# Optimization experiments

Hardware: AMD Instinct MI355X
Metric: run time of the kernel (lower is better)

## Reference

```python
import jax, jax.numpy as jnp
import numpy as np

IMG = 256      # image size implied by 8x8 grid * scale 32
THRE = 0.5
DIS = 4        # img_dislocate_size
B = 64


def _shift_map(s, size, dis):
    # Pixel-level coordinate map for the dislocated half: cell r starts at
    # max(r*s - dis, 0) (the torch while-loop clamps negative coords to 0).
    p = jnp.arange(size)
    base = jnp.maximum((p // s) * s - dis, 0)
    return base + p % s


def _cell_norm(x, g, s):
    # Per-cell (crop) min/max normalization, matching the per-crop
    # (t - min) / (max - min + 1e-5) in HeatMaptoImg.
    b = x.shape[0]
    v = x.reshape(b, 1, g, s, g, s)
    mn = v.min(axis=(3, 5), keepdims=True)
    mx = v.max(axis=(3, 5), keepdims=True)
    return ((v - mn) / (mx - mn + 1e-5)).reshape(b, 1, g * s, g * s)


def setup_inputs() -> dict:
    key = jax.random.key(0)
    ks = jax.random.split(key, 7)
    B2 = 2 * B
    return {
        "img": jax.random.uniform(ks[0], (B, 1, IMG, IMG), jnp.float32),
        "heat8": jax.random.uniform(ks[1], (B2, 1, 8, 8), jnp.float32),
        "heat16": jax.random.uniform(ks[2], (B2, 1, 16, 16), jnp.float32),
        "heat32": jax.random.uniform(ks[3], (B2, 1, 32, 32), jnp.float32),
        "seg8": jax.random.uniform(ks[4], (B2, 1, IMG, IMG), jnp.float32),
        "seg16": jax.random.uniform(ks[5], (B2, 1, IMG, IMG), jnp.float32),
        "seg32": jax.random.uniform(ks[6], (B2, 1, IMG, IMG), jnp.float32),
    }


def reference(img, heat8, heat16, heat32, seg8, seg16, seg32):
    Bv = img.shape[0]
    label = jnp.zeros((Bv, 1, IMG, IMG), img.dtype)
    cnt = jnp.zeros_like(label)
    crops = {}
    # fine grid (scale 8) processed first, matching the reversed loop order
    for heat, seg, g in ((heat32, seg32, 32), (heat16, seg16, 16), (heat8, seg8, 8)):
        s = IMG // g                      # crop / cell size for this scale
        mask = (heat > THRE).astype(img.dtype)          # (2B,1,g,g)
        mask_pix = jnp.repeat(jnp.repeat(mask, s, axis=2), s, axis=3)  # (2B,1,256,256)
        Y = _shift_map(s, IMG, DIS)
        # dislocated half crops come from the shifted image region
        img_d = img[:, :, Y[:, None], Y[None, :]]       # (B,1,256,256)
        both = jnp.concatenate([img, img_d], axis=0)    # (2B,1,256,256)
        crops[g] = _cell_norm(both, g, s) * mask_pix
        # UnitLabels: scatter-add per-crop labels + counts, then average
        ca = mask_pix[:Bv]
        label = label + ca * seg[:Bv]
        cnt = cnt + ca
        cd = mask_pix[Bv:]
        label = label.at[:, :, Y[:, None], Y[None, :]].add(cd * seg[Bv:])
        cnt = cnt.at[:, :, Y[:, None], Y[None, :]].add(cd)
    label = label / (cnt + 1e-10)
    return (crops[32], crops[16], crops[8], label)
```

## Files before the change

### kernel.cpp

```cpp
#include <hip/hip_runtime.h>

#define IMG   256
#define IMG2  65536
#define NB    64
#define NB2   128

#define NBLK_C8   2048
#define NBLK_C16  1024
#define NBLK_C32  512
#define NBLK_LBL  4096
#define NBLK_ALL  (NBLK_C8 + NBLK_C16 + NBLK_C32 + NBLK_LBL)

template <int S>
__device__ __forceinline__ void crops_cell_row(
    const float* __restrict__ img,
    const float* __restrict__ heat,
    float* __restrict__ out,
    int src, int ci,
    float (*s_red)[32][4],
    float (*s_fin)[4]) {
    constexpr int G   = IMG / S;
    constexpr int L   = (S == 8) ? 3 : (S == 16) ? 4 : 5;
    constexpr int CPL = S / 4;

    const int tid = threadIdx.x;
    const int w   = tid >> 6;
    const int l   = tid & 63;
    const int cj  = l >> (L - 2);
    const int o   = (l & (CPL - 1)) * 4;

    const int rA   = ci * S;
    const int rB   = (ci == 0) ? 0 : rA - 4;
    const int colA = cj * S + o;
    const int colB = ((cj == 0) ? 0 : cj * S - 4) + o;

    const float* __restrict__ sp = img + (size_t)src * IMG2;

    float mnA = 3.4e38f, mxA = -3.4e38f, mnB = 3.4e38f, mxB = -3.4e38f;
#pragma unroll
    for (int k = 0; k < S / 4; ++k) {
        const int r = w + 4 * k;
        const float4 a  = *(const float4*)(sp + (rA + r) * IMG + colA);
        const float4 bq = *(const float4*)(sp + (rB + r) * IMG + colB);
        mnA = fminf(mnA, fminf(fminf(a.x, a.y), fminf(a.z, a.w)));
        mxA = fmaxf(mxA, fmaxf(fmaxf(a.x, a.y), fmaxf(a.z, a.w)));
        mnB = fminf(mnB, fminf(fminf(bq.x, bq.y), fminf(bq.z, bq.w)));
        mxB = fmaxf(mxB, fmaxf(fmaxf(bq.x, bq.y), fmaxf(bq.z, bq.w)));
    }
#pragma unroll
    for (int off = 1; off < CPL; off <<= 1) {
        mnA = fminf(mnA, __shfl_xor(mnA, off, 64));
        mxA = fmaxf(mxA, __shfl_xor(mxA, off, 64));
        mnB = fminf(mnB, __shfl_xor(mnB, off, 64));
        mxB = fmaxf(mxB, __shfl_xor(mxB, off, 64));
    }
    if ((l & (CPL - 1)) == 0) {
        float* p = &s_red[w][cj][0];
        p[0] = mnA; p[1] = mxA; p[2] = mnB; p[3] = mxB;
    }
    __syncthreads();
    if (tid < G) {
        float a0 = 3.4e38f, a1 = -3.4e38f, b0 = 3.4e38f, b1 = -3.4e38f;
#pragma unroll
        for (int ww = 0; ww < 4; ++ww) {
            a0 = fminf(a0, s_red[ww][tid][0]);
            a1 = fmaxf(a1, s_red[ww][tid][1]);
            b0 = fminf(b0, s_red[ww][tid][2]);
            b1 = fmaxf(b1, s_red[ww][tid][3]);
        }
        const float hA = heat[(size_t)src * G * G + ci * G + tid];
        const float hB = heat[(size_t)(src + NB) * G * G + ci * G + tid];
        s_fin[tid][0] = a0;
        s_fin[tid][1] = (hA > 0.5f ? 1.0f : 0.0f) / (a1 - a0 + 1e-5f);
        s_fin[tid][2] = b0;
        s_fin[tid][3] = (hB > 0.5f ? 1.0f : 0.0f) / (b1 - b0 + 1e-5f);
    }
    __syncthreads();
    const float fmnA = s_fin[cj][0], finvA = s_fin[cj][1];
    const float fmnB = s_fin[cj][2], finvB = s_fin[cj][3];

    float* __restrict__ dA = out + (size_t)src * IMG2;
    float* __restrict__ dB = out + (size_t)(src + NB) * IMG2;
#pragma unroll
    for (int k = 0; k < S / 4; ++k) {
        const int r = w + 4 * k;
        const float4 a  = *(const float4*)(sp + (rA + r) * IMG + colA);
        const float4 bq = *(const float4*)(sp + (rB + r) * IMG + colB);
        float4 oa, ob;
        oa.x = (a.x - fmnA) * finvA;  oa.y = (a.y - fmnA) * finvA;
        oa.z = (a.z - fmnA) * finvA;  oa.w = (a.w - fmnA) * finvA;
        ob.x = (bq.x - fmnB) * finvB; ob.y = (bq.y - fmnB) * finvB;
        ob.z = (bq.z - fmnB) * finvB; ob.w = (bq.w - fmnB) * finvB;
        *(float4*)(dA + (rA + r) * IMG + colA) = oa;
        *(float4*)(dB + (rA + r) * IMG + colA) = ob;
    }
}

__device__ __forceinline__ void label_rows(
    const float* __restrict__ heat8,
    const float* __restrict__ heat16,
    const float* __restrict__ heat32,
    const float* __restrict__ seg8,
    const float* __restrict__ seg16,
    const float* __restrict__ seg32,
    float* __restrict__ out,
    int b, int u0) {
    const int wave = threadIdx.x >> 6;
    const int lane = threadIdx.x & 63;
    const int u    = u0 + wave;
    const int v0   = lane << 2;
    const int vs   = min(v0 + 4, 252);

    float nu[4] = {0.f, 0.f, 0.f, 0.f};
    float de[4] = {0.f, 0.f, 0.f, 0.f};

    if (u0 >= 32 && u0 <= 248) {
        const int i1 = u + 4;
#define SCALE_F(heat, seg, g, l, s)                                           \
        {                                                                     \
            const float* __restrict__ h1 = heat + b * (g * g);                \
            const float* __restrict__ h2 = heat + (NB + b) * (g * g);         \
            const float* __restrict__ r1 = seg + (size_t)b * IMG2 + u * IMG;  \
            const float* __restrict__ r2 =                                    \
                seg + (size_t)(NB + b) * IMG2 + i1 * IMG;                     \
            const float4 sd  = *(const float4*)(r1 + v0);                     \
            const float4 sg0 = *(const float4*)(r2 + v0);                     \
            const float4 sg1 = *(const float4*)(r2 + vs);                     \
            const float hd  = h1[(u >> l) * g + (v0 >> l)];                   \
            const float hg0 = h2[(i1 >> l) * g + (v0 >> l)];                  \
            const float hg1 = h2[(i1 >> l) * g + (vs >> l)];                  \
            const float md = (hd > 0.5f) ? 1.0f : 0.0f;                       \
            const float g0 = (hg0 > 0.5f) ? 1.0f : 0.0f;                      \
            const float g1 = (hg1 > 0.5f) ? 1.0f : 0.0f;                      \
            _Pragma("unroll")                                                 \
            for (int c = 0; c < 4; ++c) {                                     \
                const int v = v0 + c;                                         \
                const float m0 = (v < (s)) ? g0 : 0.0f;                       \
                const float m1 = (v >= (s) - 4 && v <= 251) ? g1 : 0.0f;      \
                float x = ((const float*)&sd)[c] * md;                        \
                x = fmaf(m0, ((const float*)&sg0)[c], x);                     \
                x = fmaf(m1, ((const float*)&sg1)[c], x);                     \
                nu[c] += x;                                                   \
                de[c] += md + m0 + m1;                                        \
            }                                                                 \
        }
        SCALE_F(heat32, seg32, 32, 3, 8)
        SCALE_F(heat16, seg16, 16, 4, 16)
        SCALE_F(heat8,  seg8,  8,  5, 32)
#undef SCALE_F
    } else {
        const int i0  = u;
        const int i1c = min(u + 4, 255);
#define SCALE_G(heat, seg, g, l, s)                                           \
        {                                                                     \
            const float* __restrict__ h1 = heat + b * (g * g);                \
            const float* __restrict__ h2 = heat + (NB + b) * (g * g);         \
            const float* __restrict__ r1 = seg + (size_t)b * IMG2 + u * IMG;  \
            const float* __restrict__ ra =                                    \
                seg + (size_t)(NB + b) * IMG2 + i0 * IMG;                     \
            const float* __restrict__ rb =                                    \
                seg + (size_t)(NB + b) * IMG2 + i1c * IMG;                    \
            const float4 sd  = *(const float4*)(r1 + v0);                     \
            const float4 a0q = *(const float4*)(ra + v0);                     \
            const float4 a1q = *(const float4*)(ra + vs);                     \
            const float4 b0q = *(const float4*)(rb + v0);                     \
            const float4 b1q = *(const float4*)(rb + vs);                     \
            const float hd  = h1[(u >> l) * g + (v0 >> l)];                   \
            const float hA0 = h2[(i0 >> l) * g + (v0 >> l)];                  \
            const float hA1 = h2[(i0 >> l) * g + (vs >> l)];                  \
            const float hB0 = h2[(i1c >> l) * g + (v0 >> l)];                 \
            const float hB1 = h2[(i1c >> l) * g + (vs >> l)];                 \
            const float miA = (u < (s)) ? 1.0f : 0.0f;                        \
            const float miB = (u >= (s) - 4 && u <= 251) ? 1.0f : 0.0f;       \
            const float md  = (hd > 0.5f) ? 1.0f : 0.0f;                      \
            const float gA0 = miA * ((hA0 > 0.5f) ? 1.0f : 0.0f);             \
            const float gA1 = miA * ((hA1 > 0.5f) ? 1.0f : 0.0f);             \
            const float gB0 = miB * ((hB0 > 0.5f) ? 1.0f : 0.0f);             \
            const float gB1 = miB * ((hB1 > 0.5f) ? 1.0f : 0.0f);             \
            _Pragma("unroll")                                                 \
            for (int c = 0; c < 4; ++c) {                                     \
                const int v = v0 + c;                                         \
                const float mj0 = (v < (s)) ? 1.0f : 0.0f;                    \
                const float mj1 = (v >= (s) - 4 && v <= 251) ? 1.0f : 0.0f;   \
                const float w00 = gA0 * mj0, w01 = gA1 * mj1;                 \
                const float w10 = gB0 * mj0, w11 = gB1 * mj1;                 \
                float x = ((const float*)&sd)[c] * md;                        \
                x = fmaf(w00, ((const float*)&a0q)[c], x);                    \
                x = fmaf(w01, ((const float*)&a1q)[c], x);                    \
                x = fmaf(w10, ((const float*)&b0q)[c], x);                    \
                x = fmaf(w11, ((const float*)&b1q)[c], x);                    \
                nu[c] += x;                                                   \
                de[c] += md + w00 + w01 + w10 + w11;                          \
            }                                                                 \
        }
        SCALE_G(heat32, seg32, 32, 3, 8)
        SCALE_G(heat16, seg16, 16, 4, 16)
        SCALE_G(heat8,  seg8,  8,  5, 32)
#undef SCALE_G
    }

    float4 o;
    o.x = nu[0] / (de[0] + 1e-10f);
    o.y = nu[1] / (de[1] + 1e-10f);
    o.z = nu[2] / (de[2] + 1e-10f);
    o.w = nu[3] / (de[3] + 1e-10f);
    *(float4*)(out + (size_t)b * IMG2 + u * IMG + v0) = o;
}

__global__ __launch_bounds__(256) void fused_kernel(
    const float* __restrict__ img,
    const float* __restrict__ heat8,
    const float* __restrict__ heat16,
    const float* __restrict__ heat32,
    const float* __restrict__ seg8,
    const float* __restrict__ seg16,
    const float* __restrict__ seg32,
    float* __restrict__ out) {
    __shared__ float s_red[4][32][4];
    __shared__ float s_fin[32][4];

    float* crops32 = out;
    float* crops16 = out + (size_t)NB2 * IMG2;
    float* crops8  = out + (size_t)2 * NB2 * IMG2;
    float* label   = out + (size_t)3 * NB2 * IMG2;

    const int bid = blockIdx.x;
    if (bid < NBLK_C8) {
        crops_cell_row<8>(img, heat32, crops32, bid >> 5, bid & 31, s_red, s_fin);
    } else if (bid < NBLK_C8 + NBLK_C16) {
        const int t = bid - NBLK_C8;
        crops_cell_row<16>(img, heat16, crops16, t >> 4, t & 15, s_red, s_fin);
    } else if (bid < NBLK_C8 + NBLK_C16 + NBLK_C32) {
        const int t = bid - (NBLK_C8 + NBLK_C16);
        crops_cell_row<32>(img, heat8, crops8, t >> 3, t & 7, s_red, s_fin);
    } else {
        const int t = bid - (NBLK_C8 + NBLK_C16 + NBLK_C32);
        label_rows(heat8, heat16, heat32, seg8, seg16, seg32, label,
                   t >> 6, (t & 63) << 2);
    }
}

extern "C" void kernel_launch(void* const* d_in, const int* in_sizes, int n_in,
                              void* d_out, int out_size, void* d_ws, size_t ws_size,
                              hipStream_t stream) {
    const float* img    = (const float*)d_in[0];
    const float* heat8  = (const float*)d_in[1];
    const float* heat16 = (const float*)d_in[2];
    const float* heat32 = (const float*)d_in[3];
    const float* seg8   = (const float*)d_in[4];
    const float* seg16  = (const float*)d_in[5];
    const float* seg32  = (const float*)d_in[6];

    fused_kernel<<<dim3(NBLK_ALL), 256, 0, stream>>>(
        img, heat8, heat16, heat32, seg8, seg16, seg32, (float*)d_out);
}
```

Measured before the change: 221.5 us.

## Use nontemporal stores, register-cache crop tiles, and merge label rows per block

Crop kernels for scales 8 and 16 now keep their loaded tiles in registers instead of reloading them for the normalize pass. All output writes use nontemporal stores to avoid polluting cache. Each label block now handles eight rows instead of four, which halves the label block count, and label blocks are scheduled first. Together these aim to cut redundant global reads and cache pressure in a bandwidth-bound kernel, at the cost of more registers per thread and a new block ordering.

After: 223.2 us. No clear change (+0.8%).

```diff
diff --git a/kernel.cpp b/kernel.cpp
--- a/kernel.cpp
+++ b/kernel.cpp
@@ -5,14 +5,22 @@
 #define NB    64
 #define NB2   128
 
+#define NBLK_LBL  2048
 #define NBLK_C8   2048
 #define NBLK_C16  1024
 #define NBLK_C32  512
-#define NBLK_LBL  4096
-#define NBLK_ALL  (NBLK_C8 + NBLK_C16 + NBLK_C32 + NBLK_LBL)
+#define NBLK_ALL  (NBLK_LBL + NBLK_C8 + NBLK_C16 + NBLK_C32)
+
+typedef float vfloat4 __attribute__((ext_vector_type(4)));
+
+__device__ __forceinline__ void nt_store4(float* p, float x, float y,
+                                          float z, float w) {
+    vfloat4 v = {x, y, z, w};
+    __builtin_nontemporal_store(v, (vfloat4*)p);
+}
 
 template <int S>
-__device__ __forceinline__ void crops_cell_row(
+__device__ __forceinline__ void crops_cell_row_reg(
     const float* __restrict__ img,
     const float* __restrict__ heat,
     float* __restrict__ out,
@@ -20,8 +28,9 @@
     float (*s_red)[32][4],
     float (*s_fin)[4]) {
     constexpr int G   = IMG / S;
-    constexpr int L   = (S == 8) ? 3 : (S == 16) ? 4 : 5;
+    constexpr int L   = (S == 8) ? 3 : 4;
     constexpr int CPL = S / 4;
+    constexpr int K   = S / 4;
 
     const int tid = threadIdx.x;
     const int w   = tid >> 6;
@@ -36,16 +45,20 @@
 
     const float* __restrict__ sp = img + (size_t)src * IMG2;
 
+    float4 av[K], bv[K];
     float mnA = 3.4e38f, mxA = -3.4e38f, mnB = 3.4e38f, mxB = -3.4e38f;
 #pragma unroll
-    for (int k = 0; k < S / 4; ++k) {
+    for (int k = 0; k < K; ++k) {
         const int r = w + 4 * k;
-        const float4 a  = *(const float4*)(sp + (rA + r) * IMG + colA);
-        const float4 bq = *(const float4*)(sp + (rB + r) * IMG + colB);
-        mnA = fminf(mnA, fminf(fminf(a.x, a.y), fminf(a.z, a.w)));
-        mxA = fmaxf(mxA, fmaxf(fmaxf(a.x, a.y), fmaxf(a.z, a.w)));
-        mnB = fminf(mnB, fminf(fminf(bq.x, bq.y), fminf(bq.z, bq.w)));
-        mxB = fmaxf(mxB, fmaxf(fmaxf(bq.x, bq.y), fmaxf(bq.z, bq.w)));
+        av[k] = *(const float4*)(sp + (rA + r) * IMG + colA);
+        bv[k] = *(const float4*)(sp + (rB + r) * IMG + colB);
+    }
+#pragma unroll
+    for (int k = 0; k < K; ++k) {
+        mnA = fminf(mnA, fminf(fminf(av[k].x, av[k].y), fminf(av[k].z, av[k].w)));
+        mxA = fmaxf(mxA, fmaxf(fmaxf(av[k].x, av[k].y), fmaxf(av[k].z, av[k].w)));
+        mnB = fminf(mnB, fminf(fminf(bv[k].x, bv[k].y), fminf(bv[k].z, bv[k].w)));
+        mxB = fmaxf(mxB, fmaxf(fmaxf(bv[k].x, bv[k].y), fmaxf(bv[k].z, bv[k].w)));
     }
 #pragma unroll
     for (int off = 1; off < CPL; off <<= 1) {
@@ -82,21 +95,100 @@
     float* __restrict__ dA = out + (size_t)src * IMG2;
     float* __restrict__ dB = out + (size_t)(src + NB) * IMG2;
 #pragma unroll
+    for (int k = 0; k < K; ++k) {
+        const int r = w + 4 * k;
+        nt_store4(dA + (rA + r) * IMG + colA,
+                  (av[k].x - fmnA) * finvA, (av[k].y - fmnA) * finvA,
+                  (av[k].z - fmnA) * finvA, (av[k].w - fmnA) * finvA);
+        nt_store4(dB + (rA + r) * IMG + colA,
+                  (bv[k].x - fmnB) * finvB, (bv[k].y - fmnB) * finvB,
+                  (bv[k].z - fmnB) * finvB, (bv[k].w - fmnB) * finvB);
+    }
+}
+
+__device__ __forceinline__ void crops_cell_row_32(
+    const float* __restrict__ img,
+    const float* __restrict__ heat,
+    float* __restrict__ out,
+    int src, int ci,
+    float (*s_red)[32][4],
+    float (*s_fin)[4]) {
+    constexpr int S = 32, G = 8, L = 5, CPL = 8;
+
+    const int tid = threadIdx.x;
+    const int w   = tid >> 6;
+    const int l   = tid & 63;
+    const int cj  = l >> (L - 2);
+    const int o   = (l & (CPL - 1)) * 4;
+
+    const int rA   = ci * S;
+    const int rB   = (ci == 0) ? 0 : rA - 4;
+    const int colA = cj * S + o;
+    const int colB = ((cj == 0) ? 0 : cj * S - 4) + o;
+
+    const float* __restrict__ sp = img + (size_t)src * IMG2;
+
+    float mnA = 3.4e38f, mxA = -3.4e38f, mnB = 3.4e38f, mxB = -3.4e38f;
+#pragma unroll
     for (int k = 0; k < S / 4; ++k) {
         const int r = w + 4 * k;
         const float4 a  = *(const float4*)(sp + (rA + r) * IMG + colA);
         const float4 bq = *(const float4*)(sp + (rB + r) * IMG + colB);
-        float4 oa, ob;
-        oa.x = (a.x - fmnA) * finvA;  oa.y = (a.y - fmnA) * finvA;
-        oa.z = (a.z - fmnA) * finvA;  oa.w = (a.w - fmnA) * finvA;
-        ob.x = (bq.x - fmnB) * finvB; ob.y = (bq.y - fmnB) * finvB;
-        ob.z = (bq.z - fmnB) * finvB; ob.w = (bq.w - fmnB) * finvB;
-        *(float4*)(dA + (rA + r) * IMG + colA) = oa;
-        *(float4*)(dB + (rA + r) * IMG + colA) = ob;
-    }
-}
-
-__device__ __forceinline__ void label_rows(
+        mnA = fminf(mnA, fminf(fminf(a.x, a.y), fminf(a.z, a.w)));
+        mxA = fmaxf(mxA, fmaxf(fmaxf(a.x, a.y), fmaxf(a.z, a.w)));
+        mnB = fminf(mnB, fminf(fminf(bq.x, bq.y), fminf(bq.z, bq.w)));
+        mxB = fmaxf(mxB, fmaxf(fmaxf(bq.x, bq.y), fmaxf(bq.z, bq.w)));
+    }
+#pragma unroll
+    for (int off = 1; off < CPL; off <<= 1) {
+        mnA = fminf(mnA, __shfl_xor(mnA, off, 64));
+        mxA = fmaxf(mxA, __shfl_xor(mxA, off, 64));
+        mnB = fminf(mnB, __shfl_xor(mnB, off, 64));
+        mxB = fmaxf(mxB, __shfl_xor(mxB, off, 64));
+    }
+    if ((l & (CPL - 1)) == 0) {
+        float* p = &s_red[w][cj][0];
+        p[0] = mnA; p[1] = mxA; p[2] = mnB; p[3] = mxB;
+    }
+    __syncthreads();
+    if (tid < G) {
+        float a0 = 3.4e38f, a1 = -3.4e38f, b0 = 3.4e38f, b1 = -3.4e38f;
+#pragma unroll
+        for (int ww = 0; ww < 4; ++ww) {
+            a0 = fminf(a0, s_red[ww][tid][0]);
+            a1 = fmaxf(a1, s_red[ww][tid][1]);
+            b0 = fminf(b0, s_red[ww][tid][2]);
+            b1 = fmaxf(b1, s_red[ww][tid][3]);
+        }
+        const float hA = heat[(size_t)src * G * G + ci * G + tid];
+        const float hB = heat[(size_t)(src + NB) * G * G + ci * G + tid];
+        s_fin[tid][0] = a0;
+        s_fin[tid][1] = (hA > 0.5f ? 1.0f : 0.0f) / (a1 - a0 + 1e-5f);
+        s_fin[tid][2] = b0;
+        s_fin[tid][3] = (hB > 0.5f ? 1.0f : 0.0f) / (b1 - b0 + 1e-5f);
+    }
+    __syncthreads();
+    const float fmnA = s_fin[cj][0], finvA = s_fin[cj][1];
+    const float fmnB = s_fin[cj][2], finvB = s_fin[cj][3];
+
+    float* __restrict__ dA = out + (size_t)src * IMG2;
+    float* __restrict__ dB = out + (size_t)(src + NB) * IMG2;
+#pragma unroll
+    for (int k = 0; k < S / 4; ++k) {
+        const int r = w + 4 * k;
+        const float4 a  = *(const float4*)(sp + (rA + r) * IMG + colA);
+        const float4 bq = *(const float4*)(sp + (rB + r) * IMG + colB);
+        nt_store4(dA + (rA + r) * IMG + colA,
+                  (a.x - fmnA) * finvA, (a.y - fmnA) * finvA,
+                  (a.z - fmnA) * finvA, (a.w - fmnA) * finvA);
+        nt_store4(dB + (rA + r) * IMG + colA,
+                  (bq.x - fmnB) * finvB, (bq.y - fmnB) * finvB,
+                  (bq.z - fmnB) * finvB, (bq.w - fmnB) * finvB);
+    }
+}
+
+template <bool FAST>
+__device__ __forceinline__ void label_one_row(
     const float* __restrict__ heat8,
     const float* __restrict__ heat16,
     const float* __restrict__ heat32,
@@ -104,17 +196,11 @@
     const float* __restrict__ seg16,
     const float* __restrict__ seg32,
     float* __restrict__ out,
-    int b, int u0) {
-    const int wave = threadIdx.x >> 6;
-    const int lane = threadIdx.x & 63;
-    const int u    = u0 + wave;
-    const int v0   = lane << 2;
-    const int vs   = min(v0 + 4, 252);
-
+    int b, int u, int v0, int vs) {
     float nu[4] = {0.f, 0.f, 0.f, 0.f};
     float de[4] = {0.f, 0.f, 0.f, 0.f};
 
-    if (u0 >= 32 && u0 <= 248) {
+    if constexpr (FAST) {
         const int i1 = u + 4;
 #define SCALE_F(heat, seg, g, l, s)                                           \
         {                                                                     \
@@ -199,12 +285,38 @@
 #undef SCALE_G
     }
 
-    float4 o;
-    o.x = nu[0] / (de[0] + 1e-10f);
-    o.y = nu[1] / (de[1] + 1e-10f);
-    o.z = nu[2] / (de[2] + 1e-10f);
-    o.w = nu[3] / (de[3] + 1e-10f);
-    *(float4*)(out + (size_t)b * IMG2 + u * IMG + v0) = o;
+    nt_store4(out + (size_t)b * IMG2 + u * IMG + v0,
+              nu[0] / (de[0] + 1e-10f), nu[1] / (de[1] + 1e-10f),
+              nu[2] / (de[2] + 1e-10f), nu[3] / (de[3] + 1e-10f));
+}
+
+__device__ __forceinline__ void label_rows8(
+    const float* __restrict__ heat8,
+    const float* __restrict__ heat16,
+    const float* __restrict__ heat32,
+    const float* __restrict__ seg8,
+    const float* __restrict__ seg16,
+    const float* __restrict__ seg32,
+    float* __restrict__ out,
+    int b, int u0) {
+    const int wave = threadIdx.x >> 6;
+    const int lane = threadIdx.x & 63;
+    const int v0   = lane << 2;
+    const int vs   = min(v0 + 4, 252);
+    const int uA   = u0 + wave;
+    const int uB   = u0 + 4 + wave;
+
+    if (u0 >= 32 && u0 <= 240) {
+        label_one_row<true>(heat8, heat16, heat32, seg8, seg16, seg32, out,
+                            b, uA, v0, vs);
+        label_one_row<true>(heat8, heat16, heat32, seg8, seg16, seg32, out,
+                            b, uB, v0, vs);
+    } else {
+        label_one_row<false>(heat8, heat16, heat32, seg8, seg16, seg32, out,
+                             b, uA, v0, vs);
+        label_one_row<false>(heat8, heat16, heat32, seg8, seg16, seg32, out,
+                             b, uB, v0, vs);
+    }
 }
 
 __global__ __launch_bounds__(256) void fused_kernel(
@@ -225,18 +337,18 @@
     float* label   = out + (size_t)3 * NB2 * IMG2;
 
     const int bid = blockIdx.x;
-    if (bid < NBLK_C8) {
-        crops_cell_row<8>(img, heat32, crops32, bid >> 5, bid & 31, s_red, s_fin);
-    } else if (bid < NBLK_C8 + NBLK_C16) {
-        const int t = bid - NBLK_C8;
-        crops_cell_row<16>(img, heat16, crops16, t >> 4, t & 15, s_red, s_fin);
-    } else if (bid < NBLK_C8 + NBLK_C16 + NBLK_C32) {
-        const int t = bid - (NBLK_C8 + NBLK_C16);
-        crops_cell_row<32>(img, heat8, crops8, t >> 3, t & 7, s_red, s_fin);
+    if (bid < NBLK_LBL) {
+        label_rows8(heat8, heat16, heat32, seg8, seg16, seg32, label,
+                    bid >> 5, (bid & 31) << 3);
+    } else if (bid < NBLK_LBL + NBLK_C8) {
+        const int t = bid - NBLK_LBL;
+        crops_cell_row_reg<8>(img, heat32, crops32, t >> 5, t & 31, s_red, s_fin);
+    } else if (bid < NBLK_LBL + NBLK_C8 + NBLK_C16) {
+        const int t = bid - (NBLK_LBL + NBLK_C8);
+        crops_cell_row_reg<16>(img, heat16, crops16, t >> 4, t & 15, s_red, s_fin);
     } else {
-        const int t = bid - (NBLK_C8 + NBLK_C16 + NBLK_C32);
-        label_rows(heat8, heat16, heat32, seg8, seg16, seg32, label,
-                   t >> 6, (t & 63) << 2);
+        const int t = bid - (NBLK_LBL + NBLK_C8 + NBLK_C16);
+        crops_cell_row_32(img, heat8, crops8, t >> 3, t & 7, s_red, s_fin);
     }
 }
 
```
